# Optimization experiments

Hardware: AMD Instinct MI355X
Metric: run time of the kernel (lower is better)

The kernel has to match this reference:

```python
import jax, jax.numpy as jnp
import numpy as np

_PHI = (1.0 + 5.0 ** 0.5) / 2.0
_VS = np.array([[0, 1, _PHI], [0, 1, -_PHI], [0, -1, _PHI], [0, -1, -_PHI],
                [1, _PHI, 0], [1, -_PHI, 0], [-1, _PHI, 0], [-1, -_PHI, 0],
                [_PHI, 0, 1], [_PHI, 0, -1], [-_PHI, 0, 1], [-_PHI, 0, -1]], dtype=np.float32)
_VS = _VS / np.linalg.norm(_VS, axis=-1, keepdims=True)  # 12 icosahedron vertices
_COLOR_COM = np.array([(0, 1, 2, 3, 4, 5), (0, 5, 4, 3, 2, 1), (2, 5, 4, 1, 0, 3), (5, 0, 1, 3, 2, 4),
                       (3, 5, 2, 0, 4, 1), (4, 0, 5, 2, 1, 3), (1, 3, 4, 2, 0, 5), (1, 0, 2, 4, 3, 5),
                       (4, 1, 2, 5, 0, 3), (3, 1, 4, 0, 2, 5), (5, 1, 0, 4, 2, 3), (2, 4, 5, 3, 0, 1)])
_INV = np.argsort(_COLOR_COM, axis=-1)  # inverse perms: scatter_(-1, color_com, W) == gather with _INV
_C2V = np.array([(0, 1), (6, 7), (2, 11), (4, 9), (5, 8), (3, 10)])
_ROLL = np.array([(0, 1, 2, 3, 4, 5), (0, 2, 3, 4, 5, 1), (0, 3, 4, 5, 1, 2), (0, 4, 5, 1, 2, 3), (0, 5, 1, 2, 3, 4)])
_HEADS = 8


def _build_sym(Wp):
    """(..., 18) raw params -> (..., 13, 12, 6) symmetry-expanded weights."""
    lead = Wp.shape[:-1]
    top = jnp.concatenate([Wp[..., 0:1], jnp.repeat(Wp[..., 1:2], 5, axis=-1)], axis=-1)[..., None, :]
    bot = jnp.concatenate([Wp[..., 2:3], jnp.repeat(Wp[..., 3:4], 5, axis=-1)], axis=-1)[..., None, :]
    cen = jnp.concatenate([Wp[..., 4:5], jnp.repeat(Wp[..., 5:6], 5, axis=-1)], axis=-1)[..., None, :]
    sym = Wp[..., 6:18].reshape(lead + (2, 6))[..., _ROLL].reshape(lead + (10, 6))
    W13 = jnp.concatenate([top, bot, sym, cen], axis=-2)  # (..., 13, 6)
    return W13[..., _INV]  # (..., 13, 12, 6): rotated copies via inverse color permutations


def setup_inputs() -> dict:
    key = jax.random.key(0)
    ks = jax.random.split(key, 6)
    bs, V, n, di, do = 1, 2048, 16, 32, 64
    s = 0.05
    return {
        "neighbor_index": jax.random.randint(ks[0], (bs, V, n), 0, V),
        "vertices": jax.random.normal(ks[1], (bs, V, 3), dtype=jnp.float32),
        "feature_map": jax.random.normal(ks[2], (bs, di, V, 6), dtype=jnp.float32),
        "W_dim": jax.random.normal(ks[3], (di + 1, di), dtype=jnp.float32) * s,
        "W": jax.random.normal(ks[4], (do, di, 18), dtype=jnp.float32) * s,
        "W_dir": jax.random.normal(ks[5], (di * _HEADS, 18), dtype=jnp.float32) * s,
    }


def reference(neighbor_index, vertices, feature_map, W_dim, W, W_dir):
    bs, V, n = neighbor_index.shape
    do, di, _ = W.shape
    H = _HEADS
    dph = di // H
    vs = jnp.asarray(_VS)
    c2v = jnp.asarray(_C2V)
    # neighbor direction (normalized)
    neigh = jax.vmap(lambda v, idx: v[idx])(vertices, neighbor_index)  # (bs,V,n,3)
    nd = neigh - vertices[:, :, None, :]
    ndn = nd / jnp.maximum(jnp.linalg.norm(nd, axis=-1, keepdims=True), 1e-12)
    # symmetry-expanded weights
    W_ro = _build_sym(W)       # (do, di, 13, 12, 6)
    Wd_ro = _build_sym(W_dir)  # (di*H, 13, 12, 6)
    # gather neighbor features: (bs, di, V, n, 6)
    nf = jax.vmap(lambda fm, idx: fm[:, idx])(feature_map, neighbor_index)
    # direction features discretized onto the 6 color axes
    de = jnp.einsum('vi,bqni->bqnv', vs, ndn)          # (bs,V,n,12)
    de = de[..., c2v].max(axis=-1)                      # (bs,V,n,6)
    cross = jnp.concatenate([nf, de[:, None]], axis=1)  # (bs, di+1, V, n, 6)
    cross = jnp.einsum('co,bcpni->bopni', W_dim, cross)  # (bs, di, V, n, 6)
    # per-head attention over neighbors
    Wdr = Wd_ro.reshape(H, di, 13, 12, 6).transpose(0, 1, 2, 4, 3)  # (h, c, k, i, r)
    act = jnp.einsum('hckir,bcpni->hbkpnr', Wdr[:, :, :12], cross) / (dph ** 0.5)
    act = jax.nn.softmax(act, axis=-2)                  # softmax over neighbors n
    cross_h = cross.reshape(bs, H, dph, V, n, 6)
    nfm = jnp.einsum('hbkpnr,bhcpni->bhckpir', act, cross_h).reshape(bs, di, 12, V, 6, 12)
    feat = jnp.einsum('dckri,bckpir->bdkpr', W_ro[:, :, :12], nfm)   # (bs,do,12,V,12)
    center = jnp.einsum('dcri,bcpi->bdpr', W_ro[:, :, 12], feature_map)  # (bs,do,V,12)
    ka = feat.sum(axis=2) + center                       # (bs,do,V,12)
    ka = ka[..., c2v].max(axis=-1)                       # (bs,do,V,6)
    return (ka, feature_map)
```

## Files before the change

kernel.cpp:

```cpp
#include <hip/hip_runtime.h>
#include <cstdint>
#include <cstddef>

#define NN 16
#define DI 32
#define DO 64

typedef short bf16x8 __attribute__((ext_vector_type(8)));
typedef short bf16x4 __attribute__((ext_vector_type(4)));
typedef float f32x4 __attribute__((ext_vector_type(4)));

#if defined(__has_builtin)
#  if __has_builtin(__builtin_amdgcn_mfma_f32_16x16x16_bf16)
#    define MFMA_K16(a, b, c) __builtin_amdgcn_mfma_f32_16x16x16_bf16(a, b, c, 0, 0, 0)
#    define HAVE_K16 1
#  elif __has_builtin(__builtin_amdgcn_mfma_f32_16x16x16bf16_1k)
#    define MFMA_K16(a, b, c) __builtin_amdgcn_mfma_f32_16x16x16bf16_1k(a, b, c, 0, 0, 0)
#    define HAVE_K16 1
#  endif
#  if __has_builtin(__builtin_amdgcn_cvt_pk_bf16_f32)
#    define HAVE_PKBF 1
#  endif
#endif

__device__ __constant__ int c_INV[12][6] = {
  {0,1,2,3,4,5},{0,5,4,3,2,1},{4,3,0,5,2,1},{1,2,4,3,5,0},
  {3,5,2,0,4,1},{1,4,3,5,0,2},{4,0,3,1,2,5},{1,0,2,4,3,5},
  {4,1,2,5,0,3},{3,1,4,0,2,5},{2,1,4,5,3,0},{4,5,0,3,1,2}};
__device__ __constant__ int c_ROLL[5][6] = {
  {0,1,2,3,4,5},{0,2,3,4,5,1},{0,3,4,5,1,2},{0,4,5,1,2,3},{0,5,1,2,3,4}};
__device__ __constant__ float c_VS[12][3] = {
  {0.f, 0.5257311121f, 0.8506508084f},
  {0.f, 0.5257311121f, -0.8506508084f},
  {0.f, -0.5257311121f, 0.8506508084f},
  {0.f, -0.5257311121f, -0.8506508084f},
  {0.5257311121f, 0.8506508084f, 0.f},
  {0.5257311121f, -0.8506508084f, 0.f},
  {-0.5257311121f, 0.8506508084f, 0.f},
  {-0.5257311121f, -0.8506508084f, 0.f},
  {0.8506508084f, 0.f, 0.5257311121f},
  {0.8506508084f, 0.f, -0.5257311121f},
  {-0.8506508084f, 0.f, 0.5257311121f},
  {-0.8506508084f, 0.f, -0.5257311121f}};
__device__ __constant__ int c_C2V[6][2] = {{0,1},{6,7},{2,11},{4,9},{5,8},{3,10}};

__device__ inline unsigned short f2bf(float f) {
  unsigned int u = __float_as_uint(f);
  unsigned int r = (u + 0x7fffu + ((u >> 16) & 1u)) >> 16;
  return (unsigned short)r;
}
__device__ inline unsigned int pk2(float a, float b) {
#ifdef HAVE_PKBF
  typedef __bf16 bf16v2 __attribute__((ext_vector_type(2)));
  union { bf16v2 v; unsigned int u; } cv;
  cv.v = __builtin_amdgcn_cvt_pk_bf16_f32(a, b);
  return cv.u;
#else
  return (unsigned int)f2bf(a) | ((unsigned int)f2bf(b) << 16);
#endif
}
__device__ inline unsigned short f2bf_fast(float a) {
  return (unsigned short)(pk2(a, a) & 0xffffu);
}

__device__ inline float sym13(const float* __restrict__ w, int k, int j) {
  if (k == 0)  return w[j == 0 ? 0 : 1];
  if (k == 1)  return w[j == 0 ? 2 : 3];
  if (k == 12) return w[j == 0 ? 4 : 5];
  int a = (k - 2) / 5, rr = (k - 2) % 5;
  return w[6 + a * 6 + c_ROLL[rr][j]];
}

__global__ __launch_bounds__(256) void k0_expand(
    const float* __restrict__ W, const float* __restrict__ Wdir,
    const float* __restrict__ fm, const float* __restrict__ Wdim,
    unsigned short* __restrict__ A_bf,
    unsigned short* __restrict__ W2k,
    unsigned short* __restrict__ Wck,
    unsigned short* __restrict__ fmTbf,
    unsigned short* __restrict__ wdB,
    float* __restrict__ out_fm, int V) {
  int idx = blockIdx.x * 256 + threadIdx.x;
  if (idx < 221184) {
    int row = idx / 192, ci = idx % 192;
    int h = row / 144, k = (row / 12) % 12, r = row % 12;
    int c = ci / 6, i = ci % 6;
    int rt = row >> 4, rl = row & 15;
    int ks = ci >> 5, q = (ci >> 3) & 3, j = ci & 7;
    A_bf[(((rt * 6 + ks) * 4 + q) * 16 + rl) * 8 + j] =
        f2bf_fast(0.5f * sym13(&Wdir[(h * 32 + c) * 18], k, c_INV[r][i]));
  } else if (idx < 1990656) {
    int e = idx - 221184;
    int kr = e / 12288, rem = e % 12288;
    int k = kr / 12, r = kr % 12, d = rem / 192, ci = rem % 192;
    int c = ci / 6, i = ci % 6;
    int ks = ci >> 5, q = (ci >> 3) & 3, j = ci & 7;
    W2k[kr * 12288 + ((ks * 4 + q) * 64 + d) * 8 + j] =
        f2bf_fast(sym13(&W[(d * 32 + c) * 18], k, c_INV[r][i]));
  } else if (idx < 2138112) {
    int e = idx - 1990656;
    int r = e / 12288, rem = e % 12288, d = rem / 192, ci = rem % 192;
    int c = ci / 6, i = ci % 6;
    int ks = ci >> 5, q = (ci >> 3) & 3, j = ci & 7;
    Wck[r * 12288 + ((ks * 4 + q) * 64 + d) * 8 + j] =
        f2bf_fast(sym13(&W[(d * 32 + c) * 18], 12, c_INV[r][i]));
  } else if (idx < 2138112 + 192 * V) {
    int e = idx - 2138112;
    int p = e / 192, ci = e % 192, c = ci / 6, i = ci % 6;
    float v = fm[(c * V + p) * 6 + i];
    fmTbf[e] = f2bf_fast(v);
    out_fm[(c * V + p) * 6 + i] = v;
  } else {
    int e = idx - (2138112 + 192 * V);
    if (e < 1024) {
      int j = e & 7, lane = (e >> 3) & 63, ot = e >> 9;
      int k = ((lane >> 4) & 3) * 8 + j;
      int o = ot * 16 + (lane & 15);
      wdB[e] = f2bf_fast(Wdim[k * 32 + o]);
    }
  }
}

__global__ __launch_bounds__(256, 4) void k12_main(
    const int* __restrict__ nbi, const float* __restrict__ verts,
    const float* __restrict__ fm, const float* __restrict__ Wdim,
    const unsigned short* __restrict__ wdB,
    const unsigned short* __restrict__ A_bf,
    unsigned short* __restrict__ nfm, int V) {
  __shared__ __align__(16) unsigned short in_bf[2][96][40];
  __shared__ __align__(16) float de_s[2][96];
  __shared__ __align__(16) unsigned short crossL[2][192][20];
  int t = threadIdx.x;
  int w = t >> 6, lane = t & 63;
  int quad = lane >> 4, col = lane & 15;
  int p0 = blockIdx.x * 2;
  int v = w & 1, hf = w >> 1;
  int p = p0 + v;

  for (int i = lane; i < 256; i += 64) {
    int n = i >> 4, c = hf * 16 + (i & 15);
    int nb = nbi[p * 16 + n];
    const float* src = fm + ((size_t)c * V + nb) * 6;
    float2 a  = *(const float2*)(src + 0);
    float2 b  = *(const float2*)(src + 2);
    float2 cd = *(const float2*)(src + 4);
    unsigned short* dst = &in_bf[v][n * 6][c];
    dst[0 * 40] = f2bf_fast(a.x);
    dst[1 * 40] = f2bf_fast(a.y);
    dst[2 * 40] = f2bf_fast(b.x);
    dst[3 * 40] = f2bf_fast(b.y);
    dst[4 * 40] = f2bf_fast(cd.x);
    dst[5 * 40] = f2bf_fast(cd.y);
  }
  if (hf == 0 && lane < 16) {
    int n = lane, nb = nbi[p * 16 + n];
    float px = verts[p * 3 + 0], py = verts[p * 3 + 1], pz = verts[p * 3 + 2];
    float qx = verts[nb * 3 + 0] - px, qy = verts[nb * 3 + 1] - py, qz = verts[nb * 3 + 2] - pz;
    float L = sqrtf(qx * qx + qy * qy + qz * qz);
    float inv = 1.0f / fmaxf(L, 1e-12f);
    qx *= inv; qy *= inv; qz *= inv;
    float de[12];
    #pragma unroll
    for (int vv = 0; vv < 12; ++vv)
      de[vv] = c_VS[vv][0] * qx + c_VS[vv][1] * qy + c_VS[vv][2] * qz;
    #pragma unroll
    for (int j = 0; j < 6; ++j)
      de_s[v][n * 6 + j] = fmaxf(de[c_C2V[j][0]], de[c_C2V[j][1]]);
  }
  __syncthreads();

  if (w < 2) {
    int vv = w;
    bf16x8 Bf[2];
    #pragma unroll
    for (int ot = 0; ot < 2; ++ot)
      Bf[ot] = *(const bf16x8*)(wdB + (size_t)(ot * 64 + lane) * 8);
    float wd32[2] = {Wdim[1024 + col], Wdim[1024 + 16 + col]};
    f32x4 D[6][2];
    #pragma unroll
    for (int mt = 0; mt < 6; ++mt) {
      bf16x8 a0 = *(const bf16x8*)&in_bf[vv][mt * 16 + col][quad * 8];
      f32x4 du = *(const f32x4*)&de_s[vv][mt * 16 + quad * 4];
      #pragma unroll
      for (int ot = 0; ot < 2; ++ot) {
        f32x4 acc = (f32x4){0.f, 0.f, 0.f, 0.f};
        acc = __builtin_amdgcn_mfma_f32_16x16x32_bf16(a0, Bf[ot], acc, 0, 0, 0);
        #pragma unroll
        for (int r = 0; r < 4; ++r)
          acc[r] = fmaf(du[r], wd32[ot], acc[r]);
        D[mt][ot] = acc;
      }
    }
    #pragma unroll
    for (int mt = 0; mt < 6; ++mt) {
      #pragma unroll
      for (int ot = 0; ot < 2; ++ot) {
        #pragma unroll
        for (int r = 0; r < 4; ++r) {
          int m = mt * 16 + quad * 4 + r;
          int n = m / 6, i = m - n * 6;
          crossL[vv][(ot * 16 + col) * 6 + i][n] = f2bf_fast(D[mt][ot][r]);
        }
      }
    }
  }
  __syncthreads();

  bf16x8 Afr[2][6];
  #pragma unroll
  for (int pi = 0; pi < 2; ++pi) {
    #pragma unroll
    for (int ks = 0; ks < 6; ++ks) {
      union { unsigned short s[8]; bf16x8 v8; } u;
      #pragma unroll
      for (int j = 0; j < 8; ++j)
        u.s[j] = crossL[pi][ks * 32 + quad * 8 + j][col];
      Afr[pi][ks] = u.v8;
    }
  }

  for (int rt = w; rt < 72; rt += 4) {
    int h = rt / 9;
    f32x4 acc[2];
    acc[0] = (f32x4){0.f, 0.f, 0.f, 0.f};
    acc[1] = (f32x4){0.f, 0.f, 0.f, 0.f};
    const unsigned short* Abase = A_bf + rt * 3072 + quad * 128 + col * 8;
    #pragma unroll
    for (int ks = 0; ks < 6; ++ks) {
      bf16x8 wf = *(const bf16x8*)(Abase + ks * 512);
      acc[0] = __builtin_amdgcn_mfma_f32_16x16x32_bf16(Afr[0][ks], wf, acc[0], 0, 0, 0);
      acc[1] = __builtin_amdgcn_mfma_f32_16x16x32_bf16(Afr[1][ks], wf, acc[1], 0, 0, 0);
    }
    int row0 = h * 24 + col;
    int row1 = min(h * 24 + 16 + col, 191);
    #pragma unroll
    for (int pi = 0; pi < 2; ++pi) {
      float v0 = acc[pi][0], v1 = acc[pi][1], v2 = acc[pi][2], v3 = acc[pi][3];
      float mx = fmaxf(fmaxf(v0, v1), fmaxf(v2, v3));
      mx = fmaxf(mx, __shfl_xor(mx, 16));
      mx = fmaxf(mx, __shfl_xor(mx, 32));
      float e0 = __expf(v0 - mx), e1 = __expf(v1 - mx);
      float e2 = __expf(v2 - mx), e3 = __expf(v3 - mx);
      float s = (e0 + e1) + (e2 + e3);
      s += __shfl_xor(s, 16);
      s += __shfl_xor(s, 32);
      float inv = __builtin_amdgcn_rcpf(s);
      unsigned int lo = pk2(e0 * inv, e1 * inv);
      unsigned int hi = pk2(e2 * inv, e3 * inv);
      f32x4 o0 = (f32x4){0.f, 0.f, 0.f, 0.f}, o1 = o0;
#ifdef HAVE_K16
      union { uint2 u; bf16x4 v4; } bcvt;
      bcvt.u = make_uint2(lo, hi);
      bf16x4 a0 = *(const bf16x4*)&crossL[pi][row0][quad * 4];
      bf16x4 a1 = *(const bf16x4*)&crossL[pi][row1][quad * 4];
      o0 = MFMA_K16(a0, bcvt.v4, o0);
      o1 = MFMA_K16(a1, bcvt.v4, o1);
#else
      int s0l = quad * 32 + col, s1l = s0l + 16;
      unsigned int b0 = (unsigned int)__shfl((int)lo, s0l);
      unsigned int b1 = (unsigned int)__shfl((int)hi, s0l);
      unsigned int b2 = (unsigned int)__shfl((int)lo, s1l);
      unsigned int b3 = (unsigned int)__shfl((int)hi, s1l);
      bool vq = (quad < 2);
      union { uint4 u; bf16x8 v8; } cvt;
      cvt.u = make_uint4(vq ? b0 : 0u, vq ? b1 : 0u, vq ? b2 : 0u, vq ? b3 : 0u);
      union { unsigned short s[8]; bf16x8 v8; } ua0, ua1;
      #pragma unroll
      for (int j = 0; j < 8; ++j) {
        int nn = quad * 8 + j;
        ua0.s[j] = (nn < 16) ? crossL[pi][row0][nn] : (unsigned short)0;
        ua1.s[j] = (nn < 16) ? crossL[pi][row1][nn] : (unsigned short)0;
      }
      o0 = __builtin_amdgcn_mfma_f32_16x16x32_bf16(ua0.v8, cvt.v8, o0, 0, 0, 0);
      o1 = __builtin_amdgcn_mfma_f32_16x16x32_bf16(ua1.v8, cvt.v8, o1, 0, 0, 0);
#endif
      size_t rowbase = (size_t)blockIdx.x * 55296 + (size_t)(rt * 16 + col) * 48 + pi * 24;
      uint2 w0;
      w0.x = pk2(o0[0], o0[1]);
      w0.y = pk2(o0[2], o0[3]);
      *(uint2*)(nfm + rowbase + quad * 4) = w0;
      if (quad < 2) {
        uint2 w1;
        w1.x = pk2(o1[0], o1[1]);
        w1.y = pk2(o1[2], o1[3]);
        *(uint2*)(nfm + rowbase + 16 + quad * 4) = w1;
      }
    }
  }
}

__global__ __launch_bounds__(512) void k3_feat(
    const unsigned short* __restrict__ W2k,
    const unsigned short* __restrict__ Wck,
    const unsigned short* __restrict__ fmTbf,
    const unsigned short* __restrict__ nfm,
    float* __restrict__ out, int V) {
  __shared__ float red[2][3][32][64];
  int pb = blockIdx.x, j = blockIdx.y;
  int t = threadIdx.x, w = t >> 6, lane = t & 63;
  int rhalf = w >> 2, kw = w & 3;
  int r = c_C2V[j][rhalf];
  int quad = lane >> 4, col = lane & 15;
  int p0 = pb * 32;
  f32x4 acc[4][2];
  #pragma unroll
  for (int m = 0; m < 4; ++m)
    #pragma unroll
    for (int jj = 0; jj < 2; ++jj) acc[m][jj] = (f32x4){0.f, 0.f, 0.f, 0.f};

  int base24[6];
  #pragma unroll
  for (int ks = 0; ks < 6; ++ks) {
    int ci = ks * 32 + quad * 8;
    int hh = ci / 24, oo = ci - hh * 24;
    base24[ks] = hh * 6912 + oo;
  }

  int pA = p0 + col, pB = p0 + 16 + col;
  const unsigned short* Bn0 = nfm + (size_t)(pA >> 1) * 55296 + (pA & 1) * 24;
  const unsigned short* Bn1 = nfm + (size_t)(pB >> 1) * 55296 + (pB & 1) * 24;
  const unsigned short* Bc0 = fmTbf + (size_t)pA * 192;
  const unsigned short* Bc1 = fmTbf + (size_t)pB * 192;

  int nkb = (kw == 3) ? 4 : 3;
  for (int i = 0; i < nkb; ++i) {
    int kb = kw * 3 + i;
    const unsigned short* Ab;
    int kr48 = 0;
    if (kb < 12) { Ab = W2k + (size_t)(kb * 12 + r) * 12288; kr48 = (kb * 12 + r) * 48; }
    else         { Ab = Wck + (size_t)r * 12288; }
    const unsigned short* Albase = Ab + quad * 512 + col * 8;
    #pragma unroll
    for (int ks = 0; ks < 6; ++ks) {
      bf16x8 b0, b1;
      if (kb < 12) {
        b0 = *(const bf16x8*)(Bn0 + base24[ks] + kr48);
        b1 = *(const bf16x8*)(Bn1 + base24[ks] + kr48);
      } else {
        int ko = ks * 32 + quad * 8;
        b0 = *(const bf16x8*)(Bc0 + ko);
        b1 = *(const bf16x8*)(Bc1 + ko);
      }
      #pragma unroll
      for (int m = 0; m < 4; ++m) {
        bf16x8 a = *(const bf16x8*)(Albase + ks * 2048 + m * 128);
        acc[m][0] = __builtin_amdgcn_mfma_f32_16x16x32_bf16(a, b0, acc[m][0], 0, 0, 0);
        acc[m][1] = __builtin_amdgcn_mfma_f32_16x16x32_bf16(a, b1, acc[m][1], 0, 0, 0);
      }
    }
  }
  if (kw > 0) {
    #pragma unroll
    for (int m = 0; m < 4; ++m)
      #pragma unroll
      for (int jj = 0; jj < 2; ++jj)
        #pragma unroll
        for (int rr = 0; rr < 4; ++rr)
          red[rhalf][kw - 1][m * 8 + jj * 4 + rr][lane] = acc[m][jj][rr];
  }
  __syncthreads();
  if (kw == 0) {
    #pragma unroll
    for (int m = 0; m < 4; ++m)
      #pragma unroll
      for (int jj = 0; jj < 2; ++jj)
        #pragma unroll
        for (int rr = 0; rr < 4; ++rr) {
          int ri = m * 8 + jj * 4 + rr;
          acc[m][jj][rr] += red[rhalf][0][ri][lane] + red[rhalf][1][ri][lane] + red[rhalf][2][ri][lane];
        }
  }
  if (w == 4) {
    #pragma unroll
    for (int m = 0; m < 4; ++m)
      #pragma unroll
      for (int jj = 0; jj < 2; ++jj)
        #pragma unroll
        for (int rr = 0; rr < 4; ++rr)
          red[1][0][m * 8 + jj * 4 + rr][lane] = acc[m][jj][rr];
  }
  __syncthreads();
  if (w == 0) {
    #pragma unroll
    for (int m = 0; m < 4; ++m)
      #pragma unroll
      for (int jj = 0; jj < 2; ++jj)
        #pragma unroll
        for (int rr = 0; rr < 4; ++rr) {
          float v = fmaxf(acc[m][jj][rr], red[1][0][m * 8 + jj * 4 + rr][lane]);
          int d = m * 16 + quad * 4 + rr;
          int p = p0 + jj * 16 + col;
          out[((size_t)d * V + p) * 6 + j] = v;
        }
  }
}

extern "C" void kernel_launch(void* const* d_in, const int* in_sizes, int n_in,
                              void* d_out, int out_size, void* d_ws, size_t ws_size,
                              hipStream_t stream) {
  const int* nbi = (const int*)d_in[0];
  const float* verts = (const float*)d_in[1];
  const float* fm = (const float*)d_in[2];
  const float* Wdim = (const float*)d_in[3];
  const float* W = (const float*)d_in[4];
  const float* Wdir = (const float*)d_in[5];
  float* out = (float*)d_out;
  float* ws = (float*)d_ws;
  int V = in_sizes[0] / NN;

  unsigned short* A_bf  = (unsigned short*)ws;
  unsigned short* W2k   = (unsigned short*)(ws + 110592);
  unsigned short* Wck   = (unsigned short*)(ws + 995328);
  unsigned short* fmTbf = (unsigned short*)(ws + 1069056);
  size_t o = 1069056 + (size_t)96 * V;
  unsigned short* nfm = (unsigned short*)(ws + o);
  o += (size_t)13824 * V;
  unsigned short* wdB = (unsigned short*)(ws + o);

  int n0 = 2138112 + 192 * V + 1024;
  k0_expand<<<(n0 + 255) / 256, 256, 0, stream>>>(W, Wdir, fm, Wdim, A_bf, W2k, Wck, fmTbf,
                                                  wdB, out + (size_t)DO * V * 6, V);
  k12_main<<<V / 2, 256, 0, stream>>>(nbi, verts, fm, Wdim, wdB, A_bf, nfm, V);
  k3_feat<<<dim3(V / 32, 6), 512, 0, stream>>>(W2k, Wck, fmTbf, nfm, out, V);
}
```

Measured before the change: 158.1 us.

## Spread cross GEMM over all waves, prefetch attention weights, halve k3 point tile

In k12_main, all four waves now share the cross projection, each taking three m-tiles instead of two waves doing all six, and the results go straight to LDS. The attention weight fragments for the next head tile are prefetched into registers while the current one is processed. The softmax max-subtraction and its shuffles are dropped, which saves instructions but can overflow if the logits get large. k3_feat now tiles 16 points per block instead of 32, doubling the grid and halving accumulators, at the cost of reloading the weights twice as often.

```diff
diff --git a/kernel.cpp b/kernel.cpp
--- a/kernel.cpp
+++ b/kernel.cpp
@@ -169,16 +169,17 @@
   }
   __syncthreads();
 
-  if (w < 2) {
-    int vv = w;
+  {
+    int vv = w & 1;
+    int mtb = (w >> 1) * 3;
     bf16x8 Bf[2];
     #pragma unroll
     for (int ot = 0; ot < 2; ++ot)
       Bf[ot] = *(const bf16x8*)(wdB + (size_t)(ot * 64 + lane) * 8);
     float wd32[2] = {Wdim[1024 + col], Wdim[1024 + 16 + col]};
-    f32x4 D[6][2];
-    #pragma unroll
-    for (int mt = 0; mt < 6; ++mt) {
+    #pragma unroll
+    for (int mi = 0; mi < 3; ++mi) {
+      int mt = mtb + mi;
       bf16x8 a0 = *(const bf16x8*)&in_bf[vv][mt * 16 + col][quad * 8];
       f32x4 du = *(const f32x4*)&de_s[vv][mt * 16 + quad * 4];
       #pragma unroll
@@ -188,18 +189,11 @@
         #pragma unroll
         for (int r = 0; r < 4; ++r)
           acc[r] = fmaf(du[r], wd32[ot], acc[r]);
-        D[mt][ot] = acc;
-      }
-    }
-    #pragma unroll
-    for (int mt = 0; mt < 6; ++mt) {
-      #pragma unroll
-      for (int ot = 0; ot < 2; ++ot) {
         #pragma unroll
         for (int r = 0; r < 4; ++r) {
           int m = mt * 16 + quad * 4 + r;
           int n = m / 6, i = m - n * 6;
-          crossL[vv][(ot * 16 + col) * 6 + i][n] = f2bf_fast(D[mt][ot][r]);
+          crossL[vv][(ot * 16 + col) * 6 + i][n] = f2bf_fast(acc[r]);
         }
       }
     }
@@ -219,28 +213,35 @@
     }
   }
 
+  bf16x8 wf[6];
+  {
+    const unsigned short* Abase = A_bf + w * 3072 + quad * 128 + col * 8;
+    #pragma unroll
+    for (int ks = 0; ks < 6; ++ks) wf[ks] = *(const bf16x8*)(Abase + ks * 512);
+  }
   for (int rt = w; rt < 72; rt += 4) {
     int h = rt / 9;
     f32x4 acc[2];
     acc[0] = (f32x4){0.f, 0.f, 0.f, 0.f};
     acc[1] = (f32x4){0.f, 0.f, 0.f, 0.f};
-    const unsigned short* Abase = A_bf + rt * 3072 + quad * 128 + col * 8;
     #pragma unroll
     for (int ks = 0; ks < 6; ++ks) {
-      bf16x8 wf = *(const bf16x8*)(Abase + ks * 512);
-      acc[0] = __builtin_amdgcn_mfma_f32_16x16x32_bf16(Afr[0][ks], wf, acc[0], 0, 0, 0);
-      acc[1] = __builtin_amdgcn_mfma_f32_16x16x32_bf16(Afr[1][ks], wf, acc[1], 0, 0, 0);
+      acc[0] = __builtin_amdgcn_mfma_f32_16x16x32_bf16(Afr[0][ks], wf[ks], acc[0], 0, 0, 0);
+      acc[1] = __builtin_amdgcn_mfma_f32_16x16x32_bf16(Afr[1][ks], wf[ks], acc[1], 0, 0, 0);
+    }
+    bf16x8 wfn[6];
+    {
+      int rtn = min(rt + 4, 71);
+      const unsigned short* AbaseN = A_bf + rtn * 3072 + quad * 128 + col * 8;
+      #pragma unroll
+      for (int ks = 0; ks < 6; ++ks) wfn[ks] = *(const bf16x8*)(AbaseN + ks * 512);
     }
     int row0 = h * 24 + col;
     int row1 = min(h * 24 + 16 + col, 191);
     #pragma unroll
     for (int pi = 0; pi < 2; ++pi) {
-      float v0 = acc[pi][0], v1 = acc[pi][1], v2 = acc[pi][2], v3 = acc[pi][3];
-      float mx = fmaxf(fmaxf(v0, v1), fmaxf(v2, v3));
-      mx = fmaxf(mx, __shfl_xor(mx, 16));
-      mx = fmaxf(mx, __shfl_xor(mx, 32));
-      float e0 = __expf(v0 - mx), e1 = __expf(v1 - mx);
-      float e2 = __expf(v2 - mx), e3 = __expf(v3 - mx);
+      float e0 = __expf(acc[pi][0]), e1 = __expf(acc[pi][1]);
+      float e2 = __expf(acc[pi][2]), e3 = __expf(acc[pi][3]);
       float s = (e0 + e1) + (e2 + e3);
       s += __shfl_xor(s, 16);
       s += __shfl_xor(s, 32);
@@ -264,12 +265,12 @@
       bool vq = (quad < 2);
       union { uint4 u; bf16x8 v8; } cvt;
       cvt.u = make_uint4(vq ? b0 : 0u, vq ? b1 : 0u, vq ? b2 : 0u, vq ? b3 : 0u);
-      union { unsigned short s[8]; bf16x8 v8; } ua0, ua1;
+      union { unsigned short sv[8]; bf16x8 v8; } ua0, ua1;
       #pragma unroll
       for (int j = 0; j < 8; ++j) {
         int nn = quad * 8 + j;
-        ua0.s[j] = (nn < 16) ? crossL[pi][row0][nn] : (unsigned short)0;
-        ua1.s[j] = (nn < 16) ? crossL[pi][row1][nn] : (unsigned short)0;
+        ua0.sv[j] = (nn < 16) ? crossL[pi][row0][nn] : (unsigned short)0;
+        ua1.sv[j] = (nn < 16) ? crossL[pi][row1][nn] : (unsigned short)0;
       }
       o0 = __builtin_amdgcn_mfma_f32_16x16x32_bf16(ua0.v8, cvt.v8, o0, 0, 0, 0);
       o1 = __builtin_amdgcn_mfma_f32_16x16x32_bf16(ua1.v8, cvt.v8, o1, 0, 0, 0);
@@ -286,6 +287,8 @@
         *(uint2*)(nfm + rowbase + 16 + quad * 4) = w1;
       }
     }
+    #pragma unroll
+    for (int ks = 0; ks < 6; ++ks) wf[ks] = wfn[ks];
   }
 }
 
@@ -295,18 +298,16 @@
     const unsigned short* __restrict__ fmTbf,
     const unsigned short* __restrict__ nfm,
     float* __restrict__ out, int V) {
-  __shared__ float red[2][3][32][64];
+  __shared__ float red[2][3][16][64];
   int pb = blockIdx.x, j = blockIdx.y;
   int t = threadIdx.x, w = t >> 6, lane = t & 63;
   int rhalf = w >> 2, kw = w & 3;
   int r = c_C2V[j][rhalf];
   int quad = lane >> 4, col = lane & 15;
-  int p0 = pb * 32;
-  f32x4 acc[4][2];
+  int p0 = pb * 16;
+  f32x4 acc[4];
   #pragma unroll
-  for (int m = 0; m < 4; ++m)
-    #pragma unroll
-    for (int jj = 0; jj < 2; ++jj) acc[m][jj] = (f32x4){0.f, 0.f, 0.f, 0.f};
+  for (int m = 0; m < 4; ++m) acc[m] = (f32x4){0.f, 0.f, 0.f, 0.f};
 
   int base24[6];
   #pragma unroll
@@ -316,11 +317,9 @@
     base24[ks] = hh * 6912 + oo;
   }
 
-  int pA = p0 + col, pB = p0 + 16 + col;
+  int pA = p0 + col;
   const unsigned short* Bn0 = nfm + (size_t)(pA >> 1) * 55296 + (pA & 1) * 24;
-  const unsigned short* Bn1 = nfm + (size_t)(pB >> 1) * 55296 + (pB & 1) * 24;
   const unsigned short* Bc0 = fmTbf + (size_t)pA * 192;
-  const unsigned short* Bc1 = fmTbf + (size_t)pB * 192;
 
   int nkb = (kw == 3) ? 4 : 3;
   for (int i = 0; i < nkb; ++i) {
@@ -332,20 +331,16 @@
     const unsigned short* Albase = Ab + quad * 512 + col * 8;
     #pragma unroll
     for (int ks = 0; ks < 6; ++ks) {
-      bf16x8 b0, b1;
+      bf16x8 b0;
       if (kb < 12) {
         b0 = *(const bf16x8*)(Bn0 + base24[ks] + kr48);
-        b1 = *(const bf16x8*)(Bn1 + base24[ks] + kr48);
       } else {
-        int ko = ks * 32 + quad * 8;
-        b0 = *(const bf16x8*)(Bc0 + ko);
-        b1 = *(const bf16x8*)(Bc1 + ko);
+        b0 = *(const bf16x8*)(Bc0 + ks * 32 + quad * 8);
       }
       #pragma unroll
       for (int m = 0; m < 4; ++m) {
         bf16x8 a = *(const bf16x8*)(Albase + ks * 2048 + m * 128);
-        acc[m][0] = __builtin_amdgcn_mfma_f32_16x16x32_bf16(a, b0, acc[m][0], 0, 0, 0);
-        acc[m][1] = __builtin_amdgcn_mfma_f32_16x16x32_bf16(a, b1, acc[m][1], 0, 0, 0);
+        acc[m] = __builtin_amdgcn_mfma_f32_16x16x32_bf16(a, b0, acc[m], 0, 0, 0);
       }
     }
   }
@@ -353,45 +348,36 @@
     #pragma unroll
     for (int m = 0; m < 4; ++m)
       #pragma unroll
-      for (int jj = 0; jj < 2; ++jj)
-        #pragma unroll
-        for (int rr = 0; rr < 4; ++rr)
-          red[rhalf][kw - 1][m * 8 + jj * 4 + rr][lane] = acc[m][jj][rr];
+      for (int rr = 0; rr < 4; ++rr)
+        red[rhalf][kw - 1][m * 4 + rr][lane] = acc[m][rr];
   }
   __syncthreads();
   if (kw == 0) {
     #pragma unroll
     for (int m = 0; m < 4; ++m)
       #pragma unroll
-      for (int jj = 0; jj < 2; ++jj)
-        #pragma unroll
-        for (int rr = 0; rr < 4; ++rr) {
-          int ri = m * 8 + jj * 4 + rr;
-          acc[m][jj][rr] += red[rhalf][0][ri][lane] + red[rhalf][1][ri][lane] + red[rhalf][2][ri][lane];
-        }
+      for (int rr = 0; rr < 4; ++rr) {
+        int ri = m * 4 + rr;
+        acc[m][rr] += red[rhalf][0][ri][lane] + red[rhalf][1][ri][lane] + red[rhalf][2][ri][lane];
+      }
   }
   if (w == 4) {
     #pragma unroll
     for (int m = 0; m < 4; ++m)
       #pragma unroll
-      for (int jj = 0; jj < 2; ++jj)
-        #pragma unroll
-        for (int rr = 0; rr < 4; ++rr)
-          red[1][0][m * 8 + jj * 4 + rr][lane] = acc[m][jj][rr];
+      for (int rr = 0; rr < 4; ++rr)
+        red[1][0][m * 4 + rr][lane] = acc[m][rr];
   }
   __syncthreads();
   if (w == 0) {
     #pragma unroll
     for (int m = 0; m < 4; ++m)
       #pragma unroll
-      for (int jj = 0; jj < 2; ++jj)
-        #pragma unroll
-        for (int rr = 0; rr < 4; ++rr) {
-          float v = fmaxf(acc[m][jj][rr], red[1][0][m * 8 + jj * 4 + rr][lane]);
-          int d = m * 16 + quad * 4 + rr;
-          int p = p0 + jj * 16 + col;
-          out[((size_t)d * V + p) * 6 + j] = v;
-        }
+      for (int rr = 0; rr < 4; ++rr) {
+        float vmax = fmaxf(acc[m][rr], red[1][0][m * 4 + rr][lane]);
+        int d = m * 16 + quad * 4 + rr;
+        out[((size_t)d * V + p0 + col) * 6 + j] = vmax;
+      }
   }
 }
 
@@ -421,5 +407,5 @@
   k0_expand<<<(n0 + 255) / 256, 256, 0, stream>>>(W, Wdir, fm, Wdim, A_bf, W2k, Wck, fmTbf,
                                                   wdB, out + (size_t)DO * V * 6, V);
   k12_main<<<V / 2, 256, 0, stream>>>(nbi, verts, fm, Wdim, wdB, A_bf, nfm, V);
-  k3_feat<<<dim3(V / 32, 6), 512, 0, stream>>>(W2k, Wck, fmTbf, nfm, out, V);
-}
+  k3_feat<<<dim3(V / 16, 6), 512, 0, stream>>>(W2k, Wck, fmTbf, nfm, out, V);
+}
```

Result: no change. 157.1 us (-0.6%).
